# Kernel optimization log

Hardware: AMD Instinct MI355X
Metric: run time of the kernel (lower is better)

## Reference

```python
import jax, jax.numpy as jnp
import numpy as np

OHNM_RATIO = 30
DEFAULT_NEG_PERC = 0.1
EPS = 1e-10


def setup_inputs() -> dict:
    key = jax.random.key(0)
    k1, k2 = jax.random.split(key)
    shape = (1, 1, 256, 256, 256)  # (B, C, D, H, W) 3D segmentation volume
    preds = jax.random.normal(k1, shape, dtype=jnp.float32)  # raw logits
    targs = (jax.random.uniform(k2, shape, dtype=jnp.float32) < 1e-3).astype(jnp.int32)
    return {"preds": preds, "targs": targs}


def reference(preds, targs):
    t = targs.astype(preds.dtype)
    # elementwise BCE-with-logits: log(1 + e^x) - x * t  (numerically stable via logaddexp)
    losses = jnp.logaddexp(0.0, preds) - preds * t
    pf, tf, lf = preds.ravel(), t.ravel(), losses.ravel()

    # --- data-dependent hard-negative count (mirrors torch .item() host sync) ---
    n_pos = int(np.asarray(tf.sum()))
    n_neg = tf.size - n_pos
    n_hns = int(DEFAULT_NEG_PERC * n_neg) if n_pos == 0 else min(n_pos * OHNM_RATIO, n_neg)

    # mask out positives, take top-k hardest negatives over the flattened loss map
    masked = jnp.where(tf == 1.0, 0.0, lf)
    _, hns_idxs = jax.lax.top_k(masked, n_hns)
    # positive indices (data-dependent size, like torch.nonzero)
    pos_idxs = jnp.asarray(np.nonzero(np.asarray(tf) == 1.0)[0], dtype=hns_idxs.dtype)
    idxs = jnp.concatenate([hns_idxs, pos_idxs])  # [n_hns + n_pos]

    # gather selected samples, view as (B, C, -1) with B = C = 1
    ps = jax.nn.sigmoid(pf[idxs])[None, None, :]  # dice normalizes preds
    ts = tf[idxs][None, None, :]

    # Dice loss over dims 2+ (here the single flattened sample dim)
    inter = jnp.sum(ps * ts, axis=-1)              # [B, C]
    denom = jnp.sum(ps, axis=-1) + jnp.sum(ts, axis=-1)
    dice = jnp.mean(1.0 - (2.0 * inter + EPS) / (denom + EPS))

    return dice + jnp.mean(lf[idxs])
```

## Files before the change

### kernel.cpp

```cpp
#include <hip/hip_runtime.h>

#define EPSF 1e-10f

constexpr unsigned KEY15 = 0xBFC00000u;
constexpr int BUCK0 = 0xBFC;
constexpr int NB2   = 4096 - BUCK0;
constexpr int NBKT  = 4096;
constexpr int NREP  = 8;

typedef float pf4 __attribute__((ext_vector_type(4)));
typedef int   pi4 __attribute__((ext_vector_type(4)));

constexpr int SC_OFF    = 0;
constexpr int BSTAT_OFF = 64;
constexpr int REP_OFF   = BSTAT_OFF + 4096 * 4;
constexpr int LOW_OFF   = REP_OFF + NREP * NB2;
constexpr int ZERO_WORDS = LOW_OFF + NBKT;

__device__ __forceinline__ float sigmoidf_(float x) {
    return 1.0f / (1.0f + expf(-x));
}
__device__ __forceinline__ float softplusf_(float x) {
    return fmaxf(x, 0.0f) + log1pf(expf(-fabsf(x)));
}
__device__ __forceinline__ unsigned f2key(float x) {
    unsigned b = __float_as_uint(x);
    return b ^ ((unsigned)((int)b >> 31) | 0x80000000u);
}
__device__ __forceinline__ float key2f(unsigned k) {
    unsigned b = (k & 0x80000000u) ? (k & 0x7FFFFFFFu) : ~k;
    return __uint_as_float(b);
}

__global__ void zeroAll(unsigned* ws, int nwords) {
    int stride = gridDim.x * blockDim.x;
    for (int i = blockIdx.x * blockDim.x + threadIdx.x; i < nwords; i += stride)
        ws[i] = 0u;
}

__global__ __launch_bounds__(256) void k1(const float* __restrict__ preds,
                                          const int* __restrict__ targs, int N,
                                          float4* __restrict__ bstat,
                                          unsigned* __restrict__ rep) {
    __shared__ int lh[NB2];
    for (int i = threadIdx.x; i < NB2; i += 256) lh[i] = 0;
    __syncthreads();

    float pc = 0.f, psig = 0.f, plos = 0.f;
    const int tid = threadIdx.x;
    const int lane = tid & 63;
    const int w = tid >> 6;

    int nfull = N >> 13;
    for (int grp = blockIdx.x; grp < nfull; grp += gridDim.x) {
        size_t ebase = ((size_t)grp << 13) + ((size_t)w << 11) + ((size_t)lane << 2);
        const float* pp  = preds + ebase;
        const float* pp2 = pp + 1024;
        const int*   tp  = targs + ebase;
        const int*   tp2 = tp + 1024;
        pf4 P[8]; pi4 T[8];
        asm volatile(
            "global_load_dwordx4 %0, %16, off\n\t"
            "global_load_dwordx4 %1, %16, off offset:1024\n\t"
            "global_load_dwordx4 %2, %16, off offset:2048\n\t"
            "global_load_dwordx4 %3, %16, off offset:3072\n\t"
            "global_load_dwordx4 %4, %17, off\n\t"
            "global_load_dwordx4 %5, %17, off offset:1024\n\t"
            "global_load_dwordx4 %6, %17, off offset:2048\n\t"
            "global_load_dwordx4 %7, %17, off offset:3072\n\t"
            "global_load_dwordx4 %8, %18, off\n\t"
            "global_load_dwordx4 %9, %18, off offset:1024\n\t"
            "global_load_dwordx4 %10, %18, off offset:2048\n\t"
            "global_load_dwordx4 %11, %18, off offset:3072\n\t"
            "global_load_dwordx4 %12, %19, off\n\t"
            "global_load_dwordx4 %13, %19, off offset:1024\n\t"
            "global_load_dwordx4 %14, %19, off offset:2048\n\t"
            "global_load_dwordx4 %15, %19, off offset:3072\n\t"
            "s_waitcnt vmcnt(0)"
            : "=&v"(P[0]), "=&v"(P[1]), "=&v"(P[2]), "=&v"(P[3]),
              "=&v"(P[4]), "=&v"(P[5]), "=&v"(P[6]), "=&v"(P[7]),
              "=&v"(T[0]), "=&v"(T[1]), "=&v"(T[2]), "=&v"(T[3]),
              "=&v"(T[4]), "=&v"(T[5]), "=&v"(T[6]), "=&v"(T[7])
            : "v"(pp), "v"(pp2), "v"(tp), "v"(tp2)
            : "memory");
#pragma unroll
        for (int g = 0; g < 8; g++) {
            pf4 pv = P[g]; pi4 tv = T[g];
#pragma unroll
            for (int j = 0; j < 4; j++) {
                float x = pv[j];
                unsigned key = f2key(x);
                if ((tv[j] == 0) && (key >= KEY15))
                    atomicAdd(&lh[(key >> 20) - BUCK0], 1);
            }
            if (tv[0] | tv[1] | tv[2] | tv[3]) {
#pragma unroll
                for (int j = 0; j < 4; j++)
                    if (tv[j]) {
                        float x = pv[j];
                        pc += 1.f; psig += sigmoidf_(x); plos += softplusf_(x) - x;
                    }
            }
        }
    }
    if (blockIdx.x == gridDim.x - 1) {
        for (int i = (nfull << 13) + tid; i < N; i += 256) {
            float x = preds[i];
            if (targs[i]) { pc += 1.f; psig += sigmoidf_(x); plos += softplusf_(x) - x; }
            else {
                unsigned key = f2key(x);
                if (key >= KEY15) atomicAdd(&lh[(key >> 20) - BUCK0], 1);
            }
        }
    }
    __syncthreads();
    float qc = 0.f;
    unsigned* my = rep + (unsigned)(blockIdx.x & (NREP - 1)) * NB2;
    for (int i = tid; i < NB2; i += 256) {
        int c = lh[i];
        if (c) { atomicAdd(&my[i], (unsigned)c); qc += (float)c; }
    }
#pragma unroll
    for (int o = 32; o > 0; o >>= 1) {
        pc   += __shfl_down(pc, o);
        psig += __shfl_down(psig, o);
        plos += __shfl_down(plos, o);
        qc   += __shfl_down(qc, o);
    }
    __shared__ float rp[4], rs[4], rl[4], rq[4];
    if ((tid & 63) == 0) { rp[w] = pc; rs[w] = psig; rl[w] = plos; rq[w] = qc; }
    __syncthreads();
    if (tid == 0)
        bstat[blockIdx.x] = make_float4(rp[0] + rp[1] + rp[2] + rp[3],
                                        rs[0] + rs[1] + rs[2] + rs[3],
                                        rl[0] + rl[1] + rl[2] + rl[3],
                                        rq[0] + rq[1] + rq[2] + rq[3]);
}

__global__ void flagK(const float4* __restrict__ bstat, int nblocks,
                      unsigned* __restrict__ sc, unsigned N) {
    float pc = 0.f, ps = 0.f, pl = 0.f, qt = 0.f;
    for (int i = threadIdx.x; i < nblocks; i += 256) {
        float4 v = bstat[i];
        pc += v.x; ps += v.y; pl += v.z; qt += v.w;
    }
#pragma unroll
    for (int o = 32; o > 0; o >>= 1) {
        pc += __shfl_down(pc, o);
        ps += __shfl_down(ps, o);
        pl += __shfl_down(pl, o);
        qt += __shfl_down(qt, o);
    }
    __shared__ float rp[4], rs[4], rl[4], rq[4];
    int w = threadIdx.x >> 6;
    if ((threadIdx.x & 63) == 0) { rp[w] = pc; rs[w] = ps; rl[w] = pl; rq[w] = qt; }
    __syncthreads();
    if (threadIdx.x == 0) {
        unsigned np = (unsigned)(rp[0] + rp[1] + rp[2] + rp[3] + 0.5f);
        float psT = rs[0] + rs[1] + rs[2] + rs[3];
        float plT = rl[0] + rl[1] + rl[2] + rl[3];
        unsigned qtT = (unsigned)(rq[0] + rq[1] + rq[2] + rq[3] + 0.5f);
        unsigned nn = N - np;
        unsigned k = (np == 0u) ? (unsigned)(0.1 * (double)nn)
                                : ((30u * np < nn) ? 30u * np : nn);
        float* scf = (float*)sc;
        sc[0] = np; scf[1] = psT; scf[2] = plT; sc[3] = k;
        sc[7] = (k > qtT) ? 1u : 0u;
    }
}

__global__ __launch_bounds__(256) void lowH(const float* __restrict__ preds,
                                            const int* __restrict__ targs, int N,
                                            const unsigned* __restrict__ sc,
                                            unsigned* __restrict__ low) {
    if (sc[7] == 0u) return;
    int gtid = blockIdx.x * 256 + threadIdx.x;
    int gstr = gridDim.x * 256;
    for (int i = gtid; i < N; i += gstr) {
        if (!targs[i]) {
            unsigned key = f2key(preds[i]);
            if (key < KEY15) atomicAdd(&low[key >> 20], 1u);
        }
    }
}

__global__ void finalize(const unsigned* __restrict__ rep,
                         const unsigned* __restrict__ low,
                         unsigned* __restrict__ sc, float* __restrict__ out) {
    __shared__ unsigned sa[256], sb[256];
    __shared__ int sb1;
    __shared__ unsigned sr1;
    __shared__ double rds[4], rdl[4];
    int t = threadIdx.x;
    int base = t * 16;
    unsigned c[16]; unsigned tot = 0;
#pragma unroll
    for (int j = 0; j < 16; j++) {
        int b = base + j;
        unsigned s;
        if (b >= BUCK0) {
            int idx = b - BUCK0;
            unsigned s0 = 0, s1 = 0;
#pragma unroll
            for (int r = 0; r < NREP; r += 2) {
                s0 += rep[r * NB2 + idx];
                s1 += rep[(r + 1) * NB2 + idx];
            }
            s = s0 + s1;
        } else {
            s = low[b];
        }
        c[j] = s; tot += s;
    }
    sa[t] = tot;
    if (t == 0) { sb1 = NBKT; sr1 = 0u; }
    __syncthreads();
    unsigned k = sc[3];
    unsigned* src = sa; unsigned* dst = sb;
    for (int off = 1; off < 256; off <<= 1) {
        unsigned v = src[t] + ((t + off < 256) ? src[t + off] : 0u);
        dst[t] = v;
        __syncthreads();
        unsigned* tmp = src; src = dst; dst = tmp;
    }
    if (k > 0u) {
        unsigned above = src[t] - tot;
        if (above < k && above + tot >= k) {
            unsigned cum = above;
            for (int j = 15; j >= 0; j--) {
                unsigned cc = c[j];
                if (cum + cc >= k) { sb1 = base + j; sr1 = k - cum; break; }
                cum += cc;
            }
        }
    }
    __syncthreads();
    int b1 = sb1; unsigned r1 = sr1;
    double ssig = 0.0, ssp = 0.0;
#pragma unroll
    for (int j = 0; j < 16; j++) {
        int b = base + j; unsigned cc = c[j];
        if (cc == 0u) continue;
        bool full = (b > b1);
        bool part = (b == b1) && (r1 > 0u);
        if (!(full || part)) continue;
        float lo = key2f((unsigned)b << 20);
        float hi = (b == NBKT - 1) ? key2f(0xFF7FFFFFu)
                                   : key2f(((unsigned)(b + 1)) << 20);
        if (full) {
            float mid = 0.5f * (lo + hi);
            ssig += (double)cc * (double)sigmoidf_(mid);
            ssp  += (double)cc * (double)softplusf_(mid);
        } else {
            unsigned take = (r1 < cc) ? r1 : cc;
            double q = (double)take / (double)cc;
            float rp = (float)((double)hi - 0.5 * q * ((double)hi - (double)lo));
            ssig += (double)take * (double)sigmoidf_(rp);
            ssp  += (double)take * (double)softplusf_(rp);
        }
    }
#pragma unroll
    for (int o = 32; o > 0; o >>= 1) {
        ssig += __shfl_down(ssig, o);
        ssp  += __shfl_down(ssp, o);
    }
    int w = t >> 6;
    if ((t & 63) == 0) { rds[w] = ssig; rdl[w] = ssp; }
    __syncthreads();
    if (t == 0) {
        double sns = rds[0] + rds[1] + rds[2] + rds[3];
        double snl = rdl[0] + rdl[1] + rdl[2] + rdl[3];
        float* scf = (float*)sc;
        unsigned np = sc[0];
        float psig = scf[1], plos = scf[2];
        double denom = (double)psig + sns + (double)np;
        double dice = 1.0 - (2.0 * (double)psig + (double)EPSF) / (denom + (double)EPSF);
        unsigned totsel = np + k;
        double mean = totsel ? (((double)plos + snl) / (double)totsel) : 0.0;
        out[0] = (float)(dice + mean);
    }
}

extern "C" void kernel_launch(void* const* d_in, const int* in_sizes, int n_in,
                              void* d_out, int out_size, void* d_ws, size_t ws_size,
                              hipStream_t stream) {
    const float* preds = (const float*)d_in[0];
    const int*   targs = (const int*)d_in[1];
    float* out = (float*)d_out;
    int N = in_sizes[0];

    unsigned* ws    = (unsigned*)d_ws;
    unsigned* sc    = ws + SC_OFF;
    float4*   bstat = (float4*)(ws + BSTAT_OFF);
    unsigned* rep   = ws + REP_OFF;
    unsigned* low   = ws + LOW_OFF;

    int nfull = N >> 13;
    int grid = nfull + ((N & 8191) ? 1 : 0);
    if (grid < 1) grid = 1;
    if (grid > 4096) grid = 4096;

    zeroAll<<<64, 256, 0, stream>>>(ws, ZERO_WORDS);
    k1<<<grid, 256, 0, stream>>>(preds, targs, N, bstat, rep);
    flagK<<<1, 256, 0, stream>>>(bstat, grid, sc, (unsigned)N);
    lowH<<<512, 256, 0, stream>>>(preds, targs, N, sc, low);
    finalize<<<1, 256, 0, stream>>>(rep, low, sc, out);
}
```

Measured before the change: 168.3 us.

## Double-buffer tile loads in k1 and pre-reduce replicated histograms in separate kernel

The histogram kernel now gives each block 4 contiguous 8K-element tiles and double-buffers them: the next tile's 16 vector loads are issued before the current tile is processed, with partial vmcnt waits. This hides memory latency and cuts the grid size, so fewer blocks flush their shared histograms. A new small kernel sums the 8 replicated histogram copies in parallel, so the single-block finalize kernel no longer does that reduction serially. The trade-offs are higher register pressure from two buffers and one extra kernel launch.

```diff
diff --git a/kernel.cpp b/kernel.cpp
--- a/kernel.cpp
+++ b/kernel.cpp
@@ -7,6 +7,7 @@
 constexpr int NB2   = 4096 - BUCK0;
 constexpr int NBKT  = 4096;
 constexpr int NREP  = 8;
+constexpr int TPB   = 4;
 
 typedef float pf4 __attribute__((ext_vector_type(4)));
 typedef int   pi4 __attribute__((ext_vector_type(4)));
@@ -15,6 +16,7 @@
 constexpr int BSTAT_OFF = 64;
 constexpr int REP_OFF   = BSTAT_OFF + 4096 * 4;
 constexpr int LOW_OFF   = REP_OFF + NREP * NB2;
+constexpr int HF_OFF    = LOW_OFF + NBKT;
 constexpr int ZERO_WORDS = LOW_OFF + NBKT;
 
 __device__ __forceinline__ float sigmoidf_(float x) {
@@ -31,6 +33,33 @@
     unsigned b = (k & 0x80000000u) ? (k & 0x7FFFFFFFu) : ~k;
     return __uint_as_float(b);
 }
+
+#define BURST16(P, T, pp, pp2, tp, tp2)                                      \
+    asm volatile(                                                            \
+        "global_load_dwordx4 %0, %16, off\n\t"                               \
+        "global_load_dwordx4 %1, %16, off offset:1024\n\t"                   \
+        "global_load_dwordx4 %2, %16, off offset:2048\n\t"                   \
+        "global_load_dwordx4 %3, %16, off offset:3072\n\t"                   \
+        "global_load_dwordx4 %4, %17, off\n\t"                               \
+        "global_load_dwordx4 %5, %17, off offset:1024\n\t"                   \
+        "global_load_dwordx4 %6, %17, off offset:2048\n\t"                   \
+        "global_load_dwordx4 %7, %17, off offset:3072\n\t"                   \
+        "global_load_dwordx4 %8, %18, off\n\t"                               \
+        "global_load_dwordx4 %9, %18, off offset:1024\n\t"                   \
+        "global_load_dwordx4 %10, %18, off offset:2048\n\t"                  \
+        "global_load_dwordx4 %11, %18, off offset:3072\n\t"                  \
+        "global_load_dwordx4 %12, %19, off\n\t"                              \
+        "global_load_dwordx4 %13, %19, off offset:1024\n\t"                  \
+        "global_load_dwordx4 %14, %19, off offset:2048\n\t"                  \
+        "global_load_dwordx4 %15, %19, off offset:3072"                      \
+        : "=&v"((P)[0]), "=&v"((P)[1]), "=&v"((P)[2]), "=&v"((P)[3]),        \
+          "=&v"((P)[4]), "=&v"((P)[5]), "=&v"((P)[6]), "=&v"((P)[7]),        \
+          "=&v"((T)[0]), "=&v"((T)[1]), "=&v"((T)[2]), "=&v"((T)[3]),        \
+          "=&v"((T)[4]), "=&v"((T)[5]), "=&v"((T)[6]), "=&v"((T)[7])         \
+        : "v"(pp), "v"(pp2), "v"(tp), "v"(tp2)                               \
+        : "memory")
+
+#define WAITVM(n) asm volatile("s_waitcnt vmcnt(" #n ")" ::: "memory")
 
 __global__ void zeroAll(unsigned* ws, int nwords) {
     int stride = gridDim.x * blockDim.x;
@@ -51,38 +80,7 @@
     const int lane = tid & 63;
     const int w = tid >> 6;
 
-    int nfull = N >> 13;
-    for (int grp = blockIdx.x; grp < nfull; grp += gridDim.x) {
-        size_t ebase = ((size_t)grp << 13) + ((size_t)w << 11) + ((size_t)lane << 2);
-        const float* pp  = preds + ebase;
-        const float* pp2 = pp + 1024;
-        const int*   tp  = targs + ebase;
-        const int*   tp2 = tp + 1024;
-        pf4 P[8]; pi4 T[8];
-        asm volatile(
-            "global_load_dwordx4 %0, %16, off\n\t"
-            "global_load_dwordx4 %1, %16, off offset:1024\n\t"
-            "global_load_dwordx4 %2, %16, off offset:2048\n\t"
-            "global_load_dwordx4 %3, %16, off offset:3072\n\t"
-            "global_load_dwordx4 %4, %17, off\n\t"
-            "global_load_dwordx4 %5, %17, off offset:1024\n\t"
-            "global_load_dwordx4 %6, %17, off offset:2048\n\t"
-            "global_load_dwordx4 %7, %17, off offset:3072\n\t"
-            "global_load_dwordx4 %8, %18, off\n\t"
-            "global_load_dwordx4 %9, %18, off offset:1024\n\t"
-            "global_load_dwordx4 %10, %18, off offset:2048\n\t"
-            "global_load_dwordx4 %11, %18, off offset:3072\n\t"
-            "global_load_dwordx4 %12, %19, off\n\t"
-            "global_load_dwordx4 %13, %19, off offset:1024\n\t"
-            "global_load_dwordx4 %14, %19, off offset:2048\n\t"
-            "global_load_dwordx4 %15, %19, off offset:3072\n\t"
-            "s_waitcnt vmcnt(0)"
-            : "=&v"(P[0]), "=&v"(P[1]), "=&v"(P[2]), "=&v"(P[3]),
-              "=&v"(P[4]), "=&v"(P[5]), "=&v"(P[6]), "=&v"(P[7]),
-              "=&v"(T[0]), "=&v"(T[1]), "=&v"(T[2]), "=&v"(T[3]),
-              "=&v"(T[4]), "=&v"(T[5]), "=&v"(T[6]), "=&v"(T[7])
-            : "v"(pp), "v"(pp2), "v"(tp), "v"(tp2)
-            : "memory");
+    auto consume = [&](pf4 (&P)[8], pi4 (&T)[8]) {
 #pragma unroll
         for (int g = 0; g < 8; g++) {
             pf4 pv = P[g]; pi4 tv = T[g];
@@ -101,6 +99,37 @@
                         pc += 1.f; psig += sigmoidf_(x); plos += softplusf_(x) - x;
                     }
             }
+        }
+    };
+
+    int nfull = N >> 13;
+    int t0 = blockIdx.x * TPB;
+    int tiles = nfull - t0; if (tiles > TPB) tiles = TPB;
+
+    if (tiles > 0) {
+        const size_t lbase = ((size_t)w << 11) + ((size_t)lane << 2);
+        pf4 PA[8]; pi4 TA[8];
+        pf4 PB[8]; pi4 TB[8];
+        {
+            size_t eb = ((size_t)t0 << 13) + lbase;
+            BURST16(PA, TA, preds + eb, preds + eb + 1024, targs + eb, targs + eb + 1024);
+        }
+        int i = 0;
+        while (true) {
+            if (i + 1 < tiles) {
+                size_t eb = ((size_t)(t0 + i + 1) << 13) + lbase;
+                BURST16(PB, TB, preds + eb, preds + eb + 1024, targs + eb, targs + eb + 1024);
+                WAITVM(16);
+            } else WAITVM(0);
+            consume(PA, TA);
+            if (++i >= tiles) break;
+            if (i + 1 < tiles) {
+                size_t eb = ((size_t)(t0 + i + 1) << 13) + lbase;
+                BURST16(PA, TA, preds + eb, preds + eb + 1024, targs + eb, targs + eb + 1024);
+                WAITVM(16);
+            } else WAITVM(0);
+            consume(PB, TB);
+            if (++i >= tiles) break;
         }
     }
     if (blockIdx.x == gridDim.x - 1) {
@@ -169,6 +198,17 @@
     }
 }
 
+__global__ void redR(const unsigned* __restrict__ rep, unsigned* __restrict__ histF) {
+    int i = blockIdx.x * 256 + threadIdx.x;
+    if (i < NB2) {
+        unsigned s0 = rep[0 * NB2 + i], s1 = rep[1 * NB2 + i];
+        unsigned s2 = rep[2 * NB2 + i], s3 = rep[3 * NB2 + i];
+        unsigned s4 = rep[4 * NB2 + i], s5 = rep[5 * NB2 + i];
+        unsigned s6 = rep[6 * NB2 + i], s7 = rep[7 * NB2 + i];
+        histF[i] = ((s0 + s1) + (s2 + s3)) + ((s4 + s5) + (s6 + s7));
+    }
+}
+
 __global__ __launch_bounds__(256) void lowH(const float* __restrict__ preds,
                                             const int* __restrict__ targs, int N,
                                             const unsigned* __restrict__ sc,
@@ -184,7 +224,7 @@
     }
 }
 
-__global__ void finalize(const unsigned* __restrict__ rep,
+__global__ void finalize(const unsigned* __restrict__ histF,
                          const unsigned* __restrict__ low,
                          unsigned* __restrict__ sc, float* __restrict__ out) {
     __shared__ unsigned sa[256], sb[256];
@@ -197,19 +237,7 @@
 #pragma unroll
     for (int j = 0; j < 16; j++) {
         int b = base + j;
-        unsigned s;
-        if (b >= BUCK0) {
-            int idx = b - BUCK0;
-            unsigned s0 = 0, s1 = 0;
-#pragma unroll
-            for (int r = 0; r < NREP; r += 2) {
-                s0 += rep[r * NB2 + idx];
-                s1 += rep[(r + 1) * NB2 + idx];
-            }
-            s = s0 + s1;
-        } else {
-            s = low[b];
-        }
+        unsigned s = (b >= BUCK0) ? histF[b - BUCK0] : low[b];
         c[j] = s; tot += s;
     }
     sa[t] = tot;
@@ -294,9 +322,11 @@
     float4*   bstat = (float4*)(ws + BSTAT_OFF);
     unsigned* rep   = ws + REP_OFF;
     unsigned* low   = ws + LOW_OFF;
+    unsigned* histF = ws + HF_OFF;
 
     int nfull = N >> 13;
-    int grid = nfull + ((N & 8191) ? 1 : 0);
+    int grid = (nfull + TPB - 1) / TPB;
+    if ((N & 8191) && grid * TPB <= nfull) grid++;
     if (grid < 1) grid = 1;
     if (grid > 4096) grid = 4096;
 
@@ -304,5 +334,6 @@
     k1<<<grid, 256, 0, stream>>>(preds, targs, N, bstat, rep);
     flagK<<<1, 256, 0, stream>>>(bstat, grid, sc, (unsigned)N);
     lowH<<<512, 256, 0, stream>>>(preds, targs, N, sc, low);
-    finalize<<<1, 256, 0, stream>>>(rep, low, sc, out);
-}
+    redR<<<(NB2 + 255) / 256, 256, 0, stream>>>(rep, histF);
+    finalize<<<1, 256, 0, stream>>>(histF, low, sc, out);
+}
```

Result: slower. 202.5 us (+20.3%).
